# Kernel tuning notes

Measured on AMD Instinct MI355X. Metric: run time of the kernel, lower is better.

The kernel has to match this reference:

```python
import jax, jax.numpy as jnp
import numpy as np

W = 131072          # window size (number of observed frames)
J = 21              # number of joints
B = J - 1           # number of bones
F, PX, PY = 512.0, 512.0, 288.0   # pinhole intrinsics (SIZE_X=1024, SIZE_Y=576)
EPS = 1e-8
WEIGHTS = {"proj": 0.25, "lift": 0.25, "bone": 0.25, "smooth": 0.25}


def _euler_batch(roll, pitch, yaw):
    """Vectorized ZYX euler -> rotation matrices, numpy, [N,3,3]."""
    cr, sr = np.cos(roll), np.sin(roll)
    cp, sp = np.cos(pitch), np.sin(pitch)
    cy, sy = np.cos(yaw), np.sin(yaw)
    R = np.empty(roll.shape + (3, 3), np.float32)
    R[..., 0, 0] = cy * cp; R[..., 0, 1] = cy * sp * sr - sy * cr; R[..., 0, 2] = cy * sp * cr + sy * sr
    R[..., 1, 0] = sy * cp; R[..., 1, 1] = sy * sp * sr + cy * cr; R[..., 1, 2] = sy * sp * cr - cy * sr
    R[..., 2, 0] = -sp;     R[..., 2, 1] = cp * sr;                R[..., 2, 2] = cp * cr
    return R


def setup_inputs() -> dict:
    key = jax.random.key(0)
    ks = jax.random.split(key, 7)
    pose3d = jax.random.normal(ks[0], (W + 1, 3, J), jnp.float32)
    bone_2d = jax.random.normal(ks[1], (W, 2, J), jnp.float32)
    lift_dirs = jax.random.normal(ks[2], (W, 3, B), jnp.float32)
    # small proper drone rotations so the projection depth stays well away from 0
    ang = 0.05 * np.asarray(jax.random.normal(ks[3], (W, 3)))
    R_drone = jnp.asarray(_euler_batch(ang[:, 0], ang[:, 1], ang[:, 2]))
    # drone positions offset so pose - C_drone ~ +10 in every coordinate
    C_drone = 0.1 * jax.random.normal(ks[4], (W, 3, 1), jnp.float32) - 10.0
    bone_lengths = jax.random.uniform(ks[5], (B,), jnp.float32, 0.5, 1.5)
    R_cam = jnp.asarray(_euler_batch(np.zeros(1), np.full(1, np.pi / 2), np.zeros(1))[0])
    # chain skeleton: bone i connects joint i+1 -> joint i
    bone_connections = jnp.stack([jnp.arange(1, J, dtype=jnp.int32),
                                  jnp.arange(0, J - 1, dtype=jnp.int32)], axis=1)
    return {"pose3d": pose3d, "bone_2d": bone_2d, "lift_dirs": lift_dirs,
            "R_drone": R_drone, "C_drone": C_drone, "bone_lengths": bone_lengths,
            "R_cam": R_cam, "bone_connections": bone_connections}


def _forward(pose3d, bone_2d, lift_dirs, R_drone, C_drone, bone_lengths, R_cam,
             bone_connections):
    Jn = pose3d.shape[2]
    b0 = bone_connections[:, 0]
    b1 = bone_connections[:, 1]
    p = pose3d[1:]                                   # [W,3,J] frames with observations

    # ---- projection loss: cam = R_cam @ R_drone^T @ (p - C_drone), pinhole
    rel = p - C_drone                                # [W,3,J]
    cam = jnp.einsum('ij,wkj,wkn->win', R_cam, R_drone, rel)  # [W,3,J]
    z = cam[:, 2]
    proj2d = jnp.stack([F * cam[:, 0] / z + PX,
                        F * cam[:, 1] / z + PY], axis=1)       # [W,2,J]
    proj_loss = jnp.sum((proj2d - bone_2d) ** 2) / (2 * Jn)

    # ---- lift loss: unit bone direction vectors vs lifted directions
    bv = p[:, :, b0] - p[:, :, b1]                   # [W,3,B]
    dirs = bv / (jnp.linalg.norm(bv, axis=1, keepdims=True) + EPS)
    lift_loss = jnp.sum((lift_dirs - dirs) ** 2) / (3 * Jn)

    # ---- bone-length loss over all W+1 frames (squared lengths, as in torch code)
    bvall = pose3d[:, :, b0] - pose3d[:, :, b1]      # [W+1,3,B]
    blen = jnp.sum(bvall ** 2, axis=1)               # [W+1,B]
    bone_loss = jnp.sum((bone_lengths[None, :] - blen) ** 2) / (Jn - 1)

    # ---- smoothness: second difference of the pose trajectory
    d = pose3d[1:] - pose3d[:-1]                     # [W,3,J]
    smooth_loss = jnp.sum((d[1:] - d[:-1]) ** 2) / (3 * Jn)

    return (WEIGHTS["proj"] * proj_loss + WEIGHTS["lift"] * lift_loss
            + WEIGHTS["bone"] * bone_loss + WEIGHTS["smooth"] * smooth_loss)


def reference(pose3d, bone_2d, lift_dirs, R_drone, C_drone, bone_lengths, R_cam,
              bone_connections):
    return _forward(pose3d, bone_2d, lift_dirs, R_drone, C_drone, bone_lengths,
                    R_cam, bone_connections)
```

## Files before the change

### kernel.cpp

```cpp
#include <hip/hip_runtime.h>

namespace {

typedef float f2 __attribute__((ext_vector_type(2)));

constexpr int JN = 21;
constexpr int FR = 64;

constexpr float F_F  = 512.0f;
constexpr float PX_F = 512.0f;
constexpr float PY_F = 288.0f;
constexpr float EPS_F = 1e-8f;

constexpr float WPROJ   = 0.25f / (2.0f * 21.0f);
constexpr float WLIFT   = 0.25f / (3.0f * 21.0f);
constexpr float WBONE   = 0.25f / 20.0f;
constexpr float WSMOOTH = 0.25f / (3.0f * 21.0f);

__device__ __forceinline__ double block_reduce(double val) {
    __shared__ double smem[16];
    const int lane = threadIdx.x & 63;
    const int wid  = threadIdx.x >> 6;
    #pragma unroll
    for (int off = 32; off > 0; off >>= 1)
        val += __shfl_down(val, off, 64);
    if (lane == 0) smem[wid] = val;
    __syncthreads();
    if (wid == 0) {
        const int nw = blockDim.x >> 6;
        val = (lane < nw) ? smem[lane] : 0.0;
        #pragma unroll
        for (int off = 32; off > 0; off >>= 1)
            val += __shfl_down(val, off, 64);
    }
    return val;
}

__global__ __launch_bounds__(256) void pose_loss_kernel(
    const float* __restrict__ pose3d,
    const float* __restrict__ bone_2d,
    const float* __restrict__ lift_dirs,
    const float* __restrict__ R_drone,
    const float* __restrict__ C_drone,
    const float* __restrict__ bone_len,
    const float* __restrict__ R_cam,
    float* __restrict__ partials,
    int W)
{
    __shared__ alignas(16) float s_pose[(FR + 2) * 63 + 2];
    __shared__ alignas(16) float s_M[FR * 12];

    const int tid = threadIdx.x;
    const int w0  = blockIdx.x * FR;
    const int nF  = min(FR, W - w0);
    const int nPoseF = min(FR + 2, W + 1 - w0);

    {
        const float* src = pose3d + (size_t)w0 * 63;
        const int nfl = nPoseF * 63;
        const int n4 = nfl >> 2;
        const float4* s4 = (const float4*)src;
        float4* d4 = (float4*)s_pose;
        for (int i = tid; i < n4; i += 256) d4[i] = s4[i];
        for (int i = (n4 << 2) + tid; i < nfl; i += 256) s_pose[i] = src[i];
    }

    if (tid < nF) {
        const float* Rd = R_drone + (size_t)(w0 + tid) * 9;
        float rd[9];
        #pragma unroll
        for (int k = 0; k < 9; ++k) rd[k] = Rd[k];
        float rc[9];
        #pragma unroll
        for (int k = 0; k < 9; ++k) rc[k] = R_cam[k];
        float M[9];
        #pragma unroll
        for (int i = 0; i < 3; ++i)
            #pragma unroll
            for (int k = 0; k < 3; ++k)
                M[i * 3 + k] = rc[i * 3 + 0] * rd[k * 3 + 0]
                             + rc[i * 3 + 1] * rd[k * 3 + 1]
                             + rc[i * 3 + 2] * rd[k * 3 + 2];
        const float* Cp = C_drone + (size_t)(w0 + tid) * 3;
        const float C0 = Cp[0], C1 = Cp[1], C2 = Cp[2];
        float MC[3];
        #pragma unroll
        for (int i = 0; i < 3; ++i)
            MC[i] = M[i * 3 + 0] * C0 + M[i * 3 + 1] * C1 + M[i * 3 + 2] * C2;
        float* mb = s_M + tid * 12;
        mb[0] = M[0]; mb[1] = M[3];
        mb[2] = M[1]; mb[3] = M[4];
        mb[4] = M[2]; mb[5] = M[5];
        mb[6] = MC[0]; mb[7] = MC[1];
        mb[8] = M[6]; mb[9] = M[7]; mb[10] = M[8]; mb[11] = MC[2];
    }
    __syncthreads();

    float partial = 0.0f;

    if (tid < 252) {
        const int j = tid % 21;
        const int g = tid / 21;
        const bool hasBone = (j < 20);
        const float blj = hasBone ? bone_len[j] : 0.0f;

        for (int wl = g; wl < nF; wl += 12) {
            const int w = w0 + wl;
            const float* P0 = s_pose + wl * 63;
            const float* P1 = P0 + 63;
            const float* mb = s_M + wl * 12;

            const float x0 = P1[j], y0 = P1[21 + j], z0 = P1[42 + j];

            {
                const f2 A = *(const f2*)(mb + 0);
                const f2 B = *(const f2*)(mb + 2);
                const f2 C = *(const f2*)(mb + 4);
                const f2 D = *(const f2*)(mb + 6);
                const float4 E = *(const float4*)(mb + 8);
                f2 c01 = A * x0 + B * y0 + C * z0 - D;
                const float c2 = E.x * x0 + E.y * y0 + E.z * z0 - E.w;
                const float invz = __builtin_amdgcn_rcpf(c2);
                f2 uv = c01 * (F_F * invz) + (f2){PX_F, PY_F};
                const f2 b2 = { bone_2d[(size_t)w * 42 + j],
                                bone_2d[(size_t)w * 42 + 21 + j] };
                const f2 duv = uv - b2;
                partial += WPROJ * (duv.x * duv.x + duv.y * duv.y);
            }

            if (hasBone) {
                const float ax = P1[j + 1]      - x0;
                const float ay = P1[21 + j + 1] - y0;
                const float az = P1[42 + j + 1] - z0;
                const float q  = ax * ax + ay * ay + az * az;
                const float inv = __builtin_amdgcn_rcpf(
                                      __builtin_amdgcn_sqrtf(q) + EPS_F);
                const float lx = lift_dirs[(size_t)w * 60 + j]      - ax * inv;
                const float ly = lift_dirs[(size_t)w * 60 + 20 + j] - ay * inv;
                const float lz = lift_dirs[(size_t)w * 60 + 40 + j] - az * inv;
                partial += WLIFT * (lx * lx + ly * ly + lz * lz);

                const float bx = P0[j + 1]      - P0[j];
                const float by = P0[21 + j + 1] - P0[21 + j];
                const float bz = P0[42 + j + 1] - P0[42 + j];
                const float e = blj - (bx * bx + by * by + bz * bz);
                partial += WBONE * (e * e);
                if (w == W - 1) {
                    const float e2 = blj - q;
                    partial += WBONE * (e2 * e2);
                }
            }

            if (w < W - 1) {
                const float* P2 = P0 + 126;
                const float sx = P2[j]      - 2.0f * x0 + P0[j];
                const float sy = P2[21 + j] - 2.0f * y0 + P0[21 + j];
                const float sz = P2[42 + j] - 2.0f * z0 + P0[42 + j];
                partial += WSMOOTH * (sx * sx + sy * sy + sz * sz);
            }
        }
    }

    const double bsum = block_reduce((double)partial);
    if (tid == 0) partials[blockIdx.x] = (float)bsum;
}

__global__ __launch_bounds__(256) void final_reduce_kernel(
    const float* __restrict__ partials, float* __restrict__ out, int n)
{
    double v = 0.0;
    const int n4 = n >> 2;
    const float4* p4 = (const float4*)partials;
    for (int i = threadIdx.x; i < n4; i += blockDim.x) {
        const float4 x = p4[i];
        v += (double)x.x + (double)x.y + (double)x.z + (double)x.w;
    }
    for (int i = (n4 << 2) + threadIdx.x; i < n; i += blockDim.x)
        v += (double)partials[i];
    v = block_reduce(v);
    if (threadIdx.x == 0) out[0] = (float)v;
}

}

extern "C" void kernel_launch(void* const* d_in, const int* in_sizes, int n_in,
                              void* d_out, int out_size, void* d_ws, size_t ws_size,
                              hipStream_t stream) {
    const float* pose3d    = (const float*)d_in[0];
    const float* bone_2d   = (const float*)d_in[1];
    const float* lift_dirs = (const float*)d_in[2];
    const float* R_drone   = (const float*)d_in[3];
    const float* C_drone   = (const float*)d_in[4];
    const float* bone_len  = (const float*)d_in[5];
    const float* R_cam     = (const float*)d_in[6];
    float* out = (float*)d_out;
    float* partials = (float*)d_ws;

    const int W = in_sizes[3] / 9;
    const int grid = (W + FR - 1) / FR;

    pose_loss_kernel<<<grid, 256, 0, stream>>>(
        pose3d, bone_2d, lift_dirs, R_drone, C_drone, bone_len, R_cam, partials, W);
    final_reduce_kernel<<<1, 256, 0, stream>>>(partials, out, grid);
}
```

Measured before the change: 23.70 us.

## Give each thread consecutive frames with rolling register window of poses

Each thread group now processes a contiguous run of four frames instead of strided frames, keeping the previous, current and next pose rows for its joint in registers and rotating them as it advances. This cuts redundant shared-memory reads of the pose rows, and the frames per block drop from 64 to 48 so that 12 groups of 4 cover the tile. The smaller tile increases the block count and the partial-sum count, and lengthens the serial dependency chain within each thread. The shared pose buffer padding grows slightly to cover reads of the j+1 neighbour.

```diff
diff --git a/kernel.cpp b/kernel.cpp
--- a/kernel.cpp
+++ b/kernel.cpp
@@ -4,8 +4,8 @@
 
 typedef float f2 __attribute__((ext_vector_type(2)));
 
-constexpr int JN = 21;
-constexpr int FR = 64;
+constexpr int FR  = 48;
+constexpr int FPG = 4;
 
 constexpr float F_F  = 512.0f;
 constexpr float PX_F = 512.0f;
@@ -47,7 +47,7 @@
     float* __restrict__ partials,
     int W)
 {
-    __shared__ alignas(16) float s_pose[(FR + 2) * 63 + 2];
+    __shared__ alignas(16) float s_pose[(FR + 2) * 63 + 6];
     __shared__ alignas(16) float s_M[FR * 12];
 
     const int tid = threadIdx.x;
@@ -88,10 +88,8 @@
         for (int i = 0; i < 3; ++i)
             MC[i] = M[i * 3 + 0] * C0 + M[i * 3 + 1] * C1 + M[i * 3 + 2] * C2;
         float* mb = s_M + tid * 12;
-        mb[0] = M[0]; mb[1] = M[3];
-        mb[2] = M[1]; mb[3] = M[4];
-        mb[4] = M[2]; mb[5] = M[5];
-        mb[6] = MC[0]; mb[7] = MC[1];
+        mb[0] = M[0]; mb[1] = M[3]; mb[2]  = M[1]; mb[3]  = M[4];
+        mb[4] = M[2]; mb[5] = M[5]; mb[6]  = MC[0]; mb[7] = MC[1];
         mb[8] = M[6]; mb[9] = M[7]; mb[10] = M[8]; mb[11] = MC[2];
     }
     __syncthreads();
@@ -103,60 +101,68 @@
         const int g = tid / 21;
         const bool hasBone = (j < 20);
         const float blj = hasBone ? bone_len[j] : 0.0f;
-
-        for (int wl = g; wl < nF; wl += 12) {
-            const int w = w0 + wl;
-            const float* P0 = s_pose + wl * 63;
-            const float* P1 = P0 + 63;
-            const float* mb = s_M + wl * 12;
-
-            const float x0 = P1[j], y0 = P1[21 + j], z0 = P1[42 + j];
-
-            {
-                const f2 A = *(const f2*)(mb + 0);
-                const f2 B = *(const f2*)(mb + 2);
-                const f2 C = *(const f2*)(mb + 4);
-                const f2 D = *(const f2*)(mb + 6);
-                const float4 E = *(const float4*)(mb + 8);
-                f2 c01 = A * x0 + B * y0 + C * z0 - D;
-                const float c2 = E.x * x0 + E.y * y0 + E.z * z0 - E.w;
-                const float invz = __builtin_amdgcn_rcpf(c2);
-                f2 uv = c01 * (F_F * invz) + (f2){PX_F, PY_F};
-                const f2 b2 = { bone_2d[(size_t)w * 42 + j],
-                                bone_2d[(size_t)w * 42 + 21 + j] };
-                const f2 duv = uv - b2;
-                partial += WPROJ * (duv.x * duv.x + duv.y * duv.y);
-            }
-
-            if (hasBone) {
-                const float ax = P1[j + 1]      - x0;
-                const float ay = P1[21 + j + 1] - y0;
-                const float az = P1[42 + j + 1] - z0;
-                const float q  = ax * ax + ay * ay + az * az;
-                const float inv = __builtin_amdgcn_rcpf(
-                                      __builtin_amdgcn_sqrtf(q) + EPS_F);
-                const float lx = lift_dirs[(size_t)w * 60 + j]      - ax * inv;
-                const float ly = lift_dirs[(size_t)w * 60 + 20 + j] - ay * inv;
-                const float lz = lift_dirs[(size_t)w * 60 + 40 + j] - az * inv;
-                partial += WLIFT * (lx * lx + ly * ly + lz * lz);
-
-                const float bx = P0[j + 1]      - P0[j];
-                const float by = P0[21 + j + 1] - P0[21 + j];
-                const float bz = P0[42 + j + 1] - P0[42 + j];
-                const float e = blj - (bx * bx + by * by + bz * bz);
-                partial += WBONE * (e * e);
-                if (w == W - 1) {
-                    const float e2 = blj - q;
-                    partial += WBONE * (e2 * e2);
+        const int base = g * FPG;
+
+        if (base < nF) {
+            const int end = min(base + FPG, nF);
+
+            const float* Pa = s_pose + base * 63;
+            float ax0 = Pa[j],      ay0 = Pa[21 + j],      az0 = Pa[42 + j];
+            float ax1 = Pa[j + 1],  ay1 = Pa[21 + j + 1],  az1 = Pa[42 + j + 1];
+            float bx0 = Pa[63 + j],     by0 = Pa[84 + j],      bz0 = Pa[105 + j];
+            float bx1 = Pa[63 + j + 1], by1 = Pa[84 + j + 1],  bz1 = Pa[105 + j + 1];
+
+            for (int wl = base; wl < end; ++wl) {
+                const int w = w0 + wl;
+                const float* P2 = s_pose + (wl + 2) * 63;
+                const float cx0 = P2[j],     cy0 = P2[21 + j],     cz0 = P2[42 + j];
+                const float cx1 = P2[j + 1], cy1 = P2[21 + j + 1], cz1 = P2[42 + j + 1];
+
+                {
+                    const float4 q0 = *(const float4*)(s_M + wl * 12);
+                    const float4 q1 = *(const float4*)(s_M + wl * 12 + 4);
+                    const float4 q2 = *(const float4*)(s_M + wl * 12 + 8);
+                    f2 c01 = (f2){q0.x, q0.y} * bx0 + (f2){q0.z, q0.w} * by0
+                           + (f2){q1.x, q1.y} * bz0 - (f2){q1.z, q1.w};
+                    const float c2 = q2.x * bx0 + q2.y * by0 + q2.z * bz0 - q2.w;
+                    const float invz = __builtin_amdgcn_rcpf(c2);
+                    f2 uv = c01 * (F_F * invz) + (f2){PX_F, PY_F};
+                    const f2 b2 = { bone_2d[(size_t)w * 42 + j],
+                                    bone_2d[(size_t)w * 42 + 21 + j] };
+                    const f2 duv = uv - b2;
+                    partial += WPROJ * (duv.x * duv.x + duv.y * duv.y);
                 }
-            }
-
-            if (w < W - 1) {
-                const float* P2 = P0 + 126;
-                const float sx = P2[j]      - 2.0f * x0 + P0[j];
-                const float sy = P2[21 + j] - 2.0f * y0 + P0[21 + j];
-                const float sz = P2[42 + j] - 2.0f * z0 + P0[42 + j];
-                partial += WSMOOTH * (sx * sx + sy * sy + sz * sz);
+
+                if (hasBone) {
+                    const float vx = bx1 - bx0, vy = by1 - by0, vz = bz1 - bz0;
+                    const float q  = vx * vx + vy * vy + vz * vz;
+                    const float inv = __builtin_amdgcn_rcpf(
+                                          __builtin_amdgcn_sqrtf(q) + EPS_F);
+                    const float lx = lift_dirs[(size_t)w * 60 + j]      - vx * inv;
+                    const float ly = lift_dirs[(size_t)w * 60 + 20 + j] - vy * inv;
+                    const float lz = lift_dirs[(size_t)w * 60 + 40 + j] - vz * inv;
+                    partial += WLIFT * (lx * lx + ly * ly + lz * lz);
+
+                    const float ux = ax1 - ax0, uy = ay1 - ay0, uz = az1 - az0;
+                    const float e = blj - (ux * ux + uy * uy + uz * uz);
+                    partial += WBONE * (e * e);
+                    if (w == W - 1) {
+                        const float e2 = blj - q;
+                        partial += WBONE * (e2 * e2);
+                    }
+                }
+
+                if (w < W - 1) {
+                    const float sx = cx0 - 2.0f * bx0 + ax0;
+                    const float sy = cy0 - 2.0f * by0 + ay0;
+                    const float sz = cz0 - 2.0f * bz0 + az0;
+                    partial += WSMOOTH * (sx * sx + sy * sy + sz * sz);
+                }
+
+                ax0 = bx0; ay0 = by0; az0 = bz0;
+                ax1 = bx1; ay1 = by1; az1 = bz1;
+                bx0 = cx0; by0 = cy0; bz0 = cz0;
+                bx1 = cx1; by1 = cy1; bz1 = cz1;
             }
         }
     }
```

Measured after the change: 25.78 us. 1.09x slower.
